# Optimization experiments

Hardware: AMD Instinct MI355X
Metric: run time of the kernel (lower is better)

Reference implementation:

```python
import jax, jax.numpy as jnp
import numpy as np

N_NODES = 100000
N_EDGES = 1600000
C_IN = 128
C_OUT = 128


def setup_inputs() -> dict:
    key = jax.random.key(0)
    k1, k2, k3, k4, k5 = jax.random.split(key, 5)
    x = jax.random.normal(k1, (N_NODES, C_IN), dtype=jnp.float32)
    W = jax.random.normal(k2, (2 * C_IN, C_OUT), dtype=jnp.float32) * (1.0 / np.sqrt(2 * C_IN))
    b = jax.random.normal(k3, (C_OUT,), dtype=jnp.float32) * 0.01
    src = jax.random.randint(k4, (N_EDGES,), 0, N_NODES, dtype=jnp.int64 if jax.config.jax_enable_x64 else jnp.int32)
    dst = jax.random.randint(k5, (N_EDGES,), 0, N_NODES, dtype=jnp.int64 if jax.config.jax_enable_x64 else jnp.int32)
    return {"x": x, "W": W, "b": b, "src": src, "dst": dst}


def reference(x, W, b, src, dst):
    # Max-Relative graph conv: per-edge relative feature, max-aggregated per dst node.
    diff = x[dst] - x[src]                                  # [E, C]  (edge messages)
    max_diff = jax.ops.segment_max(diff, dst, num_segments=x.shape[0])  # [N, C]
    # Nodes with no incoming edges: segment_max yields -inf; zero them out.
    max_diff = jnp.where(jnp.isneginf(max_diff), jnp.zeros_like(max_diff), max_diff)
    h = jnp.concatenate([x, max_diff], axis=1)              # [N, 2C]
    return jax.nn.relu(h @ W + b)                           # Linear(2C->C_out) + ReLU
```

## Files before the change

### kernel.cpp

```cpp
#include <hip/hip_runtime.h>
#include <math.h>

#define NN 100000
#define NE 1600000
#define C 128

#define TS 4096
#define NT ((NE + TS - 1) / TS)
#define BUK ((NN + 511) >> 9)
#define NSC (BUK * NT)
#define NBS ((NSC + 2047) / 2048)
#define PREP_BLKS (NN * C / 8 / 256)
#define CONVW_BLKS (2 * C * C / 256)
#define GM 64

typedef __attribute__((ext_vector_type(8))) short   bf16x8;
typedef __attribute__((ext_vector_type(4))) float   f32x4;
typedef unsigned short ushort_t;
typedef unsigned int   uint_t;

__device__ inline ushort_t f2bf(float f) {
    union { float f; uint_t u; } a; a.f = f;
    uint_t r = a.u + 0x7fff + ((a.u >> 16) & 1);
    return (ushort_t)(r >> 16);
}

__global__ __launch_bounds__(256) void k_setup(
        const float* __restrict__ x, ushort_t* __restrict__ xh,
        const float* __restrict__ W, ushort_t* __restrict__ Wt,
        const int* __restrict__ dst, int* __restrict__ tileHistT) {
    __shared__ int h[BUK];
    const int t  = threadIdx.x;
    const int bb = blockIdx.x;
    if (bb < PREP_BLKS) {
        int i = bb * 256 + t;
        int node = i >> 4;
        int c0   = (i & 15) * 8;
        const float4* xp = (const float4*)(x + (long)i * 8);
        float4 v0 = xp[0], v1 = xp[1];
        ushort_t o[8] = { f2bf(v0.x), f2bf(v0.y), f2bf(v0.z), f2bf(v0.w),
                          f2bf(v1.x), f2bf(v1.y), f2bf(v1.z), f2bf(v1.w) };
        *(bf16x8*)(xh + (long)node * 256 + c0) = *(bf16x8*)o;
    } else if (bb < PREP_BLKS + CONVW_BLKS) {
        int i = (bb - PREP_BLKS) * 256 + t;
        int k = i >> 7, n = i & 127;
        Wt[n * 256 + k] = f2bf(W[i]);
    } else {
        const int tile = bb - PREP_BLKS - CONVW_BLKS;
        for (int i = t; i < BUK; i += 256) h[i] = 0;
        __syncthreads();
        const int base = tile * TS;
        for (int i = t; i < TS; i += 256) {
            int e = base + i;
            if (e < NE) atomicAdd(&h[dst[e] >> 9], 1);
        }
        __syncthreads();
        for (int i = t; i < BUK; i += 256) tileHistT[i * NT + tile] = h[i];
    }
}

__global__ __launch_bounds__(256) void scan_partial(const int* __restrict__ in,
                                                    int* __restrict__ out,
                                                    int* __restrict__ blocksums,
                                                    int n) {
    __shared__ int ts[256];
    const int t = threadIdx.x;
    const int base = blockIdx.x * 2048 + t * 8;
    int c[8];
    int s = 0;
    #pragma unroll
    for (int j = 0; j < 8; ++j) {
        int i = base + j;
        c[j] = (i < n) ? in[i] : 0;
        s += c[j];
    }
    ts[t] = s;
    __syncthreads();
    for (int off = 1; off < 256; off <<= 1) {
        int add = (t >= off) ? ts[t - off] : 0;
        __syncthreads();
        ts[t] += add;
        __syncthreads();
    }
    int run = (t == 0) ? 0 : ts[t - 1];
    #pragma unroll
    for (int j = 0; j < 8; ++j) {
        int i = base + j;
        if (i < n) out[i] = run;
        run += c[j];
    }
    if (t == 255) blocksums[blockIdx.x] = ts[255];
}

__global__ __launch_bounds__(64) void scan_blocksums(const int* __restrict__ blocksums,
                                                     int* __restrict__ blockbase, int nb) {
    int lane = threadIdx.x;
    int v = (lane < nb) ? blocksums[lane] : 0;
    int incl = v;
    #pragma unroll
    for (int off = 1; off < 64; off <<= 1) {
        int nbr = __shfl_up(incl, off, 64);
        if (lane >= off) incl += nbr;
    }
    if (lane < nb) blockbase[lane] = incl - v;
}

__global__ __launch_bounds__(256) void p3_scatter(const int* __restrict__ dst,
                                                  const int* __restrict__ src,
                                                  const int* __restrict__ tileScan,
                                                  const int* __restrict__ blockbase,
                                                  uint_t* __restrict__ coarse) {
    __shared__ int cur[BUK];
    const int t = threadIdx.x, tile = blockIdx.x;
    for (int i = t; i < BUK; i += 256) {
        int idx = i * NT + tile;
        cur[i] = tileScan[idx] + blockbase[idx >> 11];
    }
    __syncthreads();
    const int base = tile * TS;
    for (int i = t; i < TS; i += 256) {
        int e = base + i;
        if (e < NE) {
            int d = dst[e];
            int p = atomicAdd(&cur[d >> 9], 1);
            coarse[p] = ((uint_t)(d & 511) << 17) | (uint_t)src[e];
        }
    }
}

__global__ __launch_bounds__(256) void p4_build(const uint_t* __restrict__ coarse,
                                                const int* __restrict__ tileScan,
                                                const int* __restrict__ blockbase,
                                                int* __restrict__ offs,
                                                int* __restrict__ ssrc) {
    __shared__ int cnt[512];
    __shared__ int ts[256];
    const int b = blockIdx.x, t = threadIdx.x;
    const int n0 = b << 9;
    const int i0 = b * NT;
    const int bs = tileScan[i0] + blockbase[i0 >> 11];
    int be;
    if (b == BUK - 1) be = NE;
    else { int i1 = (b + 1) * NT; be = tileScan[i1] + blockbase[i1 >> 11]; }
    cnt[t] = 0; cnt[t + 256] = 0;
    __syncthreads();
    for (int i = bs + t; i < be; i += 256)
        atomicAdd(&cnt[(int)(coarse[i] >> 17)], 1);
    __syncthreads();
    int c0 = cnt[2 * t], c1 = cnt[2 * t + 1];
    ts[t] = c0 + c1;
    __syncthreads();
    for (int off = 1; off < 256; off <<= 1) {
        int add = (t >= off) ? ts[t - off] : 0;
        __syncthreads();
        ts[t] += add;
        __syncthreads();
    }
    int ex = (t == 0) ? 0 : ts[t - 1];
    int o0 = bs + ex, o1 = o0 + c0;
    cnt[2 * t] = o0; cnt[2 * t + 1] = o1;
    if (n0 + 2 * t < NN)     offs[n0 + 2 * t]     = o0;
    if (n0 + 2 * t + 1 < NN) offs[n0 + 2 * t + 1] = o1;
    if (b == BUK - 1 && t == 0) offs[NN] = NE;
    __syncthreads();
    for (int i = bs + t; i < be; i += 256) {
        uint_t pk = coarse[i];
        int p = atomicAdd(&cnt[(int)(pk >> 17)], 1);
        ssrc[p] = (int)(pk & 0x1FFFF);
    }
}

#define ACCQ(u)  { m[0] = fminf(m[0], __uint_as_float((u).x << 16));          \
                   m[1] = fminf(m[1], __uint_as_float((u).x & 0xffff0000u));  \
                   m[2] = fminf(m[2], __uint_as_float((u).y << 16));          \
                   m[3] = fminf(m[3], __uint_as_float((u).y & 0xffff0000u));  \
                   m[4] = fminf(m[4], __uint_as_float((u).z << 16));          \
                   m[5] = fminf(m[5], __uint_as_float((u).z & 0xffff0000u));  \
                   m[6] = fminf(m[6], __uint_as_float((u).w << 16));          \
                   m[7] = fminf(m[7], __uint_as_float((u).w & 0xffff0000u)); }

__global__ __launch_bounds__(256) void node_min_v2(
        const int* __restrict__ offs, const int* __restrict__ ssrc,
        ushort_t* __restrict__ xh) {
    const int wid  = (blockIdx.x * 256 + threadIdx.x) >> 6;
    const int lane = threadIdx.x & 63;
    if (wid >= NN) return;
    const int g = lane >> 4;
    const int s = lane & 15;
    const int beg = offs[wid], end = offs[wid + 1];
    const char* xb = (const char*)xh;
    float m[8];
    #pragma unroll
    for (int j = 0; j < 8; ++j) m[j] = INFINITY;
    int i = beg;
    for (; i + 8 <= end; i += 8) {
        int e0 = ssrc[i + g];
        int e1 = ssrc[i + 4 + g];
        uint4 a = *(const uint4*)(xb + (long)e0 * 512 + s * 16);
        uint4 bq = *(const uint4*)(xb + (long)e1 * 512 + s * 16);
        ACCQ(a);
        ACCQ(bq);
    }
    for (; i < end; i += 4) {
        int e = i + g;
        int idx = ssrc[(e < end) ? e : (end - 1)];
        uint4 a = *(const uint4*)(xb + (long)idx * 512 + s * 16);
        if (e < end) ACCQ(a);
    }
    #pragma unroll
    for (int j = 0; j < 8; ++j) {
        m[j] = fminf(m[j], __shfl_xor(m[j], 16, 64));
        m[j] = fminf(m[j], __shfl_xor(m[j], 32, 64));
    }
    if (g == 0) {
        uint4 xd = *(const uint4*)(xb + (long)wid * 512 + s * 16);
        uint_t xu[4] = { xd.x, xd.y, xd.z, xd.w };
        bool has = end > beg;
        uint4 o;
        uint_t* op = (uint_t*)&o;
        #pragma unroll
        for (int j = 0; j < 4; ++j) {
            float lo = has ? (__uint_as_float(xu[j] << 16)         - m[2 * j])     : 0.0f;
            float hi = has ? (__uint_as_float(xu[j] & 0xffff0000u) - m[2 * j + 1]) : 0.0f;
            op[j] = (uint_t)f2bf(lo) | ((uint_t)f2bf(hi) << 16);
        }
        *(uint4*)((char*)xh + (long)wid * 512 + 256 + s * 16) = o;
    }
}

__global__ __launch_bounds__(256) void gemm_mfma(
        const ushort_t* __restrict__ xh, const ushort_t* __restrict__ Wt,
        const float* __restrict__ b, float* __restrict__ out) {
    const int w    = threadIdx.x >> 6;
    const int l    = threadIdx.x & 63;
    const int wcol = w * 32;
    const int lr   = l & 15;
    const int kb   = (l >> 4) * 8;

    bf16x8 bb[2][8];
    float  bv[2];
    #pragma unroll
    for (int n = 0; n < 2; ++n) {
        int col = wcol + n * 16 + lr;
        bv[n] = b[col];
        const ushort_t* wp = Wt + (long)col * 256 + kb;
        #pragma unroll
        for (int k0 = 0; k0 < 8; ++k0)
            bb[n][k0] = *(const bf16x8*)(wp + k0 * 32);
    }

    const int mb0 = blockIdx.x * GM;
    #pragma unroll
    for (int mt = 0; mt < GM / 16; ++mt) {
        int mbase = mb0 + mt * 16;
        int arow = mbase + lr;
        if (arow >= NN) arow = NN - 1;
        const ushort_t* ap = xh + (long)arow * 256 + kb;
        bf16x8 a[8];
        #pragma unroll
        for (int k0 = 0; k0 < 8; ++k0) a[k0] = *(const bf16x8*)(ap + k0 * 32);

        f32x4 acc0 = (f32x4){0.f, 0.f, 0.f, 0.f};
        f32x4 acc1 = (f32x4){0.f, 0.f, 0.f, 0.f};
        #pragma unroll
        for (int k0 = 0; k0 < 8; ++k0) {
            acc0 = __builtin_amdgcn_mfma_f32_16x16x32_bf16(a[k0], bb[0][k0], acc0, 0, 0, 0);
            acc1 = __builtin_amdgcn_mfma_f32_16x16x32_bf16(a[k0], bb[1][k0], acc1, 0, 0, 0);
        }

        int rbase = mbase + ((l >> 4) << 2);
        int col0 = wcol + lr;
        #pragma unroll
        for (int j = 0; j < 4; ++j) {
            int r = rbase + j;
            if (r < NN) {
                out[(long)r * 128 + col0]      = fmaxf(acc0[j] + bv[0], 0.0f);
                out[(long)r * 128 + col0 + 16] = fmaxf(acc1[j] + bv[1], 0.0f);
            }
        }
    }
}

__global__ void init_neginf(float* __restrict__ p, int n) {
    int i = blockIdx.x * blockDim.x + threadIdx.x;
    if (i < n) p[i] = -INFINITY;
}

__device__ inline void amaxf(float* a, float v, float cur) {
    if (cur >= v) return;
    if (v >= 0.0f) atomicMax((int*)a, __float_as_int(v));
    else           atomicMin((unsigned int*)a, __float_as_uint(v));
}

__global__ __launch_bounds__(256) void edge_max(
        const float* __restrict__ x, const int* __restrict__ src,
        const int* __restrict__ dst, float* __restrict__ maxdiff) {
    long tid = (long)blockIdx.x * blockDim.x + threadIdx.x;
    int e = (int)(tid >> 5);
    if (e >= NE) return;
    int lane = (int)(tid & 31);
    int s = src[e], d = dst[e];
    int c0 = lane * 4;
    const float4 xd = *(const float4*)(x + (long)d * C + c0);
    const float4 xs = *(const float4*)(x + (long)s * C + c0);
    float4 df;
    df.x = xd.x - xs.x; df.y = xd.y - xs.y;
    df.z = xd.z - xs.z; df.w = xd.w - xs.w;
    float* o = maxdiff + (long)d * C + c0;
    float4 cur = *(const float4*)o;
    amaxf(o + 0, df.x, cur.x);
    amaxf(o + 1, df.y, cur.y);
    amaxf(o + 2, df.z, cur.z);
    amaxf(o + 3, df.w, cur.w);
}

#define TN 32
__global__ __launch_bounds__(256) void gemm_relu(
        const float* __restrict__ x, const float* __restrict__ W,
        const float* __restrict__ b, float* __restrict__ out) {
    __shared__ float h[TN][2 * C];
    const int nb = blockIdx.x * TN;
    const int t  = threadIdx.x;
    for (int i = t; i < TN * 2 * C / 4; i += 256) {
        int idx  = i * 4;
        int node = idx / (2 * C);
        int ci   = idx % (2 * C);
        float4 v;
        if (ci < C) {
            v = *(const float4*)(x + (long)(nb + node) * C + ci);
        } else {
            v = *(const float4*)(out + (long)(nb + node) * C + (ci - C));
            if (v.x == -INFINITY) v.x = 0.0f;
            if (v.y == -INFINITY) v.y = 0.0f;
            if (v.z == -INFINITY) v.z = 0.0f;
            if (v.w == -INFINITY) v.w = 0.0f;
        }
        *(float4*)&h[node][ci] = v;
    }
    __syncthreads();
    const int co = (t & 31) * 4;
    const int n0 = (t >> 5) * 4;
    float acc[4][4];
    #pragma unroll
    for (int i = 0; i < 4; ++i)
        #pragma unroll
        for (int j = 0; j < 4; ++j) acc[i][j] = 0.0f;
    for (int ci = 0; ci < 2 * C; ++ci) {
        float4 w = *(const float4*)(W + (long)ci * C + co);
        #pragma unroll
        for (int i = 0; i < 4; ++i) {
            float hv = h[n0 + i][ci];
            acc[i][0] = fmaf(hv, w.x, acc[i][0]);
            acc[i][1] = fmaf(hv, w.y, acc[i][1]);
            acc[i][2] = fmaf(hv, w.z, acc[i][2]);
            acc[i][3] = fmaf(hv, w.w, acc[i][3]);
        }
    }
    float4 bias = *(const float4*)(b + co);
    #pragma unroll
    for (int i = 0; i < 4; ++i) {
        float4 r;
        r.x = fmaxf(acc[i][0] + bias.x, 0.0f);
        r.y = fmaxf(acc[i][1] + bias.y, 0.0f);
        r.z = fmaxf(acc[i][2] + bias.z, 0.0f);
        r.w = fmaxf(acc[i][3] + bias.w, 0.0f);
        *(float4*)(out + (long)(nb + n0 + i) * C + co) = r;
    }
}

extern "C" void kernel_launch(void* const* d_in, const int* in_sizes, int n_in,
                              void* d_out, int out_size, void* d_ws, size_t ws_size,
                              hipStream_t stream) {
    const float* x   = (const float*)d_in[0];
    const float* W   = (const float*)d_in[1];
    const float* b   = (const float*)d_in[2];
    const int*   src = (const int*)d_in[3];
    const int*   dst = (const int*)d_in[4];
    float* out = (float*)d_out;

    size_t ints_head = (size_t)128 + NSC + (NN + 1) + NE;
    size_t head_b    = ((ints_head * 4) + 255) & ~(size_t)255;
    size_t xh_b      = (size_t)NN * 256 * 2;
    size_t wt_b      = (size_t)2 * C * C * 2;
    size_t need      = head_b + xh_b + wt_b;

    if (ws_size >= need) {
        int* blocksums = (int*)d_ws;
        int* blockbase = blocksums + 64;
        int* tileScan  = blockbase + 64;
        int* offs      = tileScan + NSC;
        int* ssrc      = offs + NN + 1;
        ushort_t* xh   = (ushort_t*)((char*)d_ws + head_b);
        ushort_t* Wt   = (ushort_t*)((char*)d_ws + head_b + xh_b);
        int*    tileHistT = ssrc;
        uint_t* coarse    = (uint_t*)d_out;

        k_setup<<<PREP_BLKS + CONVW_BLKS + NT, 256, 0, stream>>>(x, xh, W, Wt, dst, tileHistT);
        scan_partial<<<NBS, 256, 0, stream>>>(tileHistT, tileScan, blocksums, NSC);
        scan_blocksums<<<1, 64, 0, stream>>>(blocksums, blockbase, NBS);
        p3_scatter<<<NT, 256, 0, stream>>>(dst, src, tileScan, blockbase, coarse);
        p4_build<<<BUK, 256, 0, stream>>>(coarse, tileScan, blockbase, offs, ssrc);
        node_min_v2<<<NN / 4, 256, 0, stream>>>(offs, ssrc, xh);
        gemm_mfma<<<(NN + GM - 1) / GM, 256, 0, stream>>>(xh, Wt, b, out);
    } else {
        int n = NN * C;
        init_neginf<<<(n + 255) / 256, 256, 0, stream>>>(out, n);
        long threads = (long)NE * 32;
        edge_max<<<(int)((threads + 255) / 256), 256, 0, stream>>>(x, src, dst, out);
        gemm_relu<<<(NN + TN - 1) / TN, 256, 0, stream>>>(x, W, b, out);
    }
}
```

Measured before the change: 269.4 us.

## Fold blocksum scan into consumers, stage p4 edges in LDS, add nontemporal accesses

Removes the separate single-wave scan_blocksums launch by having p3_scatter and p4_build each recompute the 64-entry blocksum prefix in LDS. p4_build now caches its bucket's packed edges in a 40KB LDS buffer so the second pass reads LDS instead of re-reading global memory, with a fallback when a bucket exceeds capacity. Loads and stores in node_min, the GEMM input and the output use nontemporal hints to reduce cache pollution. The larger LDS footprint in p4_build may lower occupancy, and each scatter block repeats the small scan.

```diff
diff --git a/kernel.cpp b/kernel.cpp
--- a/kernel.cpp
+++ b/kernel.cpp
@@ -13,9 +13,11 @@
 #define PREP_BLKS (NN * C / 8 / 256)
 #define CONVW_BLKS (2 * C * C / 256)
 #define GM 64
-
-typedef __attribute__((ext_vector_type(8))) short   bf16x8;
-typedef __attribute__((ext_vector_type(4))) float   f32x4;
+#define P4CAP 10240
+
+typedef __attribute__((ext_vector_type(8))) short        bf16x8;
+typedef __attribute__((ext_vector_type(4))) float        f32x4;
+typedef __attribute__((ext_vector_type(4))) unsigned int uintx4;
 typedef unsigned short ushort_t;
 typedef unsigned int   uint_t;
 
@@ -92,29 +94,33 @@
     if (t == 255) blocksums[blockIdx.x] = ts[255];
 }
 
-__global__ __launch_bounds__(64) void scan_blocksums(const int* __restrict__ blocksums,
-                                                     int* __restrict__ blockbase, int nb) {
-    int lane = threadIdx.x;
-    int v = (lane < nb) ? blocksums[lane] : 0;
-    int incl = v;
-    #pragma unroll
-    for (int off = 1; off < 64; off <<= 1) {
-        int nbr = __shfl_up(incl, off, 64);
-        if (lane >= off) incl += nbr;
-    }
-    if (lane < nb) blockbase[lane] = incl - v;
+__device__ inline void scan_bsums_lds(const int* __restrict__ blocksums,
+                                      int* bbase, int t) {
+    if (t < 64) {
+        int v = (t < NBS) ? blocksums[t] : 0;
+        int incl = v;
+        #pragma unroll
+        for (int off = 1; off < 64; off <<= 1) {
+            int nbr = __shfl_up(incl, off, 64);
+            if (t >= off) incl += nbr;
+        }
+        bbase[t] = incl - v;
+    }
 }
 
 __global__ __launch_bounds__(256) void p3_scatter(const int* __restrict__ dst,
                                                   const int* __restrict__ src,
                                                   const int* __restrict__ tileScan,
-                                                  const int* __restrict__ blockbase,
+                                                  const int* __restrict__ blocksums,
                                                   uint_t* __restrict__ coarse) {
     __shared__ int cur[BUK];
+    __shared__ int bbase[64];
     const int t = threadIdx.x, tile = blockIdx.x;
+    scan_bsums_lds(blocksums, bbase, t);
+    __syncthreads();
     for (int i = t; i < BUK; i += 256) {
         int idx = i * NT + tile;
-        cur[i] = tileScan[idx] + blockbase[idx >> 11];
+        cur[i] = tileScan[idx] + bbase[idx >> 11];
     }
     __syncthreads();
     const int base = tile * TS;
@@ -130,22 +136,36 @@
 
 __global__ __launch_bounds__(256) void p4_build(const uint_t* __restrict__ coarse,
                                                 const int* __restrict__ tileScan,
-                                                const int* __restrict__ blockbase,
+                                                const int* __restrict__ blocksums,
                                                 int* __restrict__ offs,
                                                 int* __restrict__ ssrc) {
+    __shared__ uint_t eds[P4CAP];
     __shared__ int cnt[512];
     __shared__ int ts[256];
+    __shared__ int bbase[64];
     const int b = blockIdx.x, t = threadIdx.x;
+    scan_bsums_lds(blocksums, bbase, t);
     const int n0 = b << 9;
+    cnt[t] = 0; cnt[t + 256] = 0;
+    __syncthreads();
     const int i0 = b * NT;
-    const int bs = tileScan[i0] + blockbase[i0 >> 11];
+    const int bs = tileScan[i0] + bbase[i0 >> 11];
     int be;
     if (b == BUK - 1) be = NE;
-    else { int i1 = (b + 1) * NT; be = tileScan[i1] + blockbase[i1 >> 11]; }
-    cnt[t] = 0; cnt[t + 256] = 0;
-    __syncthreads();
-    for (int i = bs + t; i < be; i += 256)
-        atomicAdd(&cnt[(int)(coarse[i] >> 17)], 1);
+    else { int i1 = (b + 1) * NT; be = tileScan[i1] + bbase[i1 >> 11]; }
+    const int cntE = be - bs;
+    const bool fits = cntE <= P4CAP;
+
+    if (fits) {
+        for (int i = t; i < cntE; i += 256) {
+            uint_t pk = coarse[bs + i];
+            eds[i] = pk;
+            atomicAdd(&cnt[(int)(pk >> 17)], 1);
+        }
+    } else {
+        for (int i = bs + t; i < be; i += 256)
+            atomicAdd(&cnt[(int)(coarse[i] >> 17)], 1);
+    }
     __syncthreads();
     int c0 = cnt[2 * t], c1 = cnt[2 * t + 1];
     ts[t] = c0 + c1;
@@ -163,10 +183,18 @@
     if (n0 + 2 * t + 1 < NN) offs[n0 + 2 * t + 1] = o1;
     if (b == BUK - 1 && t == 0) offs[NN] = NE;
     __syncthreads();
-    for (int i = bs + t; i < be; i += 256) {
-        uint_t pk = coarse[i];
-        int p = atomicAdd(&cnt[(int)(pk >> 17)], 1);
-        ssrc[p] = (int)(pk & 0x1FFFF);
+    if (fits) {
+        for (int i = t; i < cntE; i += 256) {
+            uint_t pk = eds[i];
+            int p = atomicAdd(&cnt[(int)(pk >> 17)], 1);
+            ssrc[p] = (int)(pk & 0x1FFFF);
+        }
+    } else {
+        for (int i = bs + t; i < be; i += 256) {
+            uint_t pk = coarse[i];
+            int p = atomicAdd(&cnt[(int)(pk >> 17)], 1);
+            ssrc[p] = (int)(pk & 0x1FFFF);
+        }
     }
 }
 
@@ -194,8 +222,8 @@
     for (int j = 0; j < 8; ++j) m[j] = INFINITY;
     int i = beg;
     for (; i + 8 <= end; i += 8) {
-        int e0 = ssrc[i + g];
-        int e1 = ssrc[i + 4 + g];
+        int e0 = __builtin_nontemporal_load(&ssrc[i + g]);
+        int e1 = __builtin_nontemporal_load(&ssrc[i + 4 + g]);
         uint4 a = *(const uint4*)(xb + (long)e0 * 512 + s * 16);
         uint4 bq = *(const uint4*)(xb + (long)e1 * 512 + s * 16);
         ACCQ(a);
@@ -203,7 +231,7 @@
     }
     for (; i < end; i += 4) {
         int e = i + g;
-        int idx = ssrc[(e < end) ? e : (end - 1)];
+        int idx = __builtin_nontemporal_load(&ssrc[(e < end) ? e : (end - 1)]);
         uint4 a = *(const uint4*)(xb + (long)idx * 512 + s * 16);
         if (e < end) ACCQ(a);
     }
@@ -216,15 +244,14 @@
         uint4 xd = *(const uint4*)(xb + (long)wid * 512 + s * 16);
         uint_t xu[4] = { xd.x, xd.y, xd.z, xd.w };
         bool has = end > beg;
-        uint4 o;
-        uint_t* op = (uint_t*)&o;
+        uintx4 o;
         #pragma unroll
         for (int j = 0; j < 4; ++j) {
             float lo = has ? (__uint_as_float(xu[j] << 16)         - m[2 * j])     : 0.0f;
             float hi = has ? (__uint_as_float(xu[j] & 0xffff0000u) - m[2 * j + 1]) : 0.0f;
-            op[j] = (uint_t)f2bf(lo) | ((uint_t)f2bf(hi) << 16);
-        }
-        *(uint4*)((char*)xh + (long)wid * 512 + 256 + s * 16) = o;
+            o[j] = (uint_t)f2bf(lo) | ((uint_t)f2bf(hi) << 16);
+        }
+        __builtin_nontemporal_store(o, (uintx4*)((char*)xh + (long)wid * 512 + 256 + s * 16));
     }
 }
 
@@ -255,10 +282,11 @@
         int mbase = mb0 + mt * 16;
         int arow = mbase + lr;
         if (arow >= NN) arow = NN - 1;
-        const ushort_t* ap = xh + (long)arow * 256 + kb;
+        const bf16x8* ap = (const bf16x8*)(xh + (long)arow * 256 + kb);
         bf16x8 a[8];
         #pragma unroll
-        for (int k0 = 0; k0 < 8; ++k0) a[k0] = *(const bf16x8*)(ap + k0 * 32);
+        for (int k0 = 0; k0 < 8; ++k0)
+            a[k0] = __builtin_nontemporal_load(&ap[k0 * 4]);
 
         f32x4 acc0 = (f32x4){0.f, 0.f, 0.f, 0.f};
         f32x4 acc1 = (f32x4){0.f, 0.f, 0.f, 0.f};
@@ -274,8 +302,10 @@
         for (int j = 0; j < 4; ++j) {
             int r = rbase + j;
             if (r < NN) {
-                out[(long)r * 128 + col0]      = fmaxf(acc0[j] + bv[0], 0.0f);
-                out[(long)r * 128 + col0 + 16] = fmaxf(acc1[j] + bv[1], 0.0f);
+                __builtin_nontemporal_store(fmaxf(acc0[j] + bv[0], 0.0f),
+                                            &out[(long)r * 128 + col0]);
+                __builtin_nontemporal_store(fmaxf(acc1[j] + bv[1], 0.0f),
+                                            &out[(long)r * 128 + col0 + 16]);
             }
         }
     }
@@ -386,8 +416,7 @@
 
     if (ws_size >= need) {
         int* blocksums = (int*)d_ws;
-        int* blockbase = blocksums + 64;
-        int* tileScan  = blockbase + 64;
+        int* tileScan  = blocksums + 128;
         int* offs      = tileScan + NSC;
         int* ssrc      = offs + NN + 1;
         ushort_t* xh   = (ushort_t*)((char*)d_ws + head_b);
@@ -397,9 +426,8 @@
 
         k_setup<<<PREP_BLKS + CONVW_BLKS + NT, 256, 0, stream>>>(x, xh, W, Wt, dst, tileHistT);
         scan_partial<<<NBS, 256, 0, stream>>>(tileHistT, tileScan, blocksums, NSC);
-        scan_blocksums<<<1, 64, 0, stream>>>(blocksums, blockbase, NBS);
-        p3_scatter<<<NT, 256, 0, stream>>>(dst, src, tileScan, blockbase, coarse);
-        p4_build<<<BUK, 256, 0, stream>>>(coarse, tileScan, blockbase, offs, ssrc);
+        p3_scatter<<<NT, 256, 0, stream>>>(dst, src, tileScan, blocksums, coarse);
+        p4_build<<<BUK, 256, 0, stream>>>(coarse, tileScan, blocksums, offs, ssrc);
         node_min_v2<<<NN / 4, 256, 0, stream>>>(offs, ssrc, xh);
         gemm_mfma<<<(NN + GM - 1) / GM, 256, 0, stream>>>(xh, Wt, b, out);
     } else {
```

After: 285.5 us. +6.0%, slower.
